# Kernel optimization log

Hardware: AMD Instinct MI355X
Metric: run time of the kernel (lower is better)

## Reference

```python
import jax, jax.numpy as jnp
import numpy as np

IN_F = 4096
OUT_F = 4096
GROUPSIZE = 128
NUM_GROUPS = IN_F // GROUPSIZE  # 32


def setup_inputs() -> dict:
    key = jax.random.key(0)
    k1, k2, k3, k4 = jax.random.split(key, 4)
    x = jax.random.normal(k1, (4, 2048, IN_F), dtype=jnp.float32)
    imin = jnp.iinfo(jnp.int32).min
    imax = jnp.iinfo(jnp.int32).max
    qweight = jax.random.randint(k2, (IN_F // 8, OUT_F), imin, imax, dtype=jnp.int32)
    qzeros = jax.random.randint(k3, (NUM_GROUPS, OUT_F // 8), imin, imax, dtype=jnp.int32)
    scales = jax.random.uniform(k4, (NUM_GROUPS, OUT_F), dtype=jnp.float32,
                                minval=1e-3, maxval=2e-2)
    return {"x": x, "qweight": qweight, "qzeros": qzeros, "scales": scales}


def _unpack_rows(q):
    # q: int32 [in/8, out] -> float nibbles [in, out]; nibble i of a word is bits 4i..4i+3
    u = q.astype(jnp.uint32)
    shifts = (4 * jnp.arange(8, dtype=jnp.uint32))[None, :, None]  # [1,8,1]
    nib = (u[:, None, :] >> shifts) & jnp.uint32(0xF)              # [in/8, 8, out]
    return nib.reshape(q.shape[0] * 8, q.shape[1]).astype(jnp.float32)


def _unpack_cols(q):
    # q: int32 [g, out/8] -> float nibbles [g, out]
    u = q.astype(jnp.uint32)
    shifts = (4 * jnp.arange(8, dtype=jnp.uint32))[None, None, :]  # [1,1,8]
    nib = (u[:, :, None] >> shifts) & jnp.uint32(0xF)              # [g, out/8, 8]
    return nib.reshape(q.shape[0], q.shape[1] * 8).astype(jnp.float32)


def _dequant(qweight, qzeros, scales):
    # GPTQ dequant: w = scale[g] * (q - (z[g] + 1))
    q = _unpack_rows(qweight)                      # [IN_F, OUT_F]
    z = _unpack_cols(qzeros) + 1.0                 # [G, OUT_F]
    qg = q.reshape(NUM_GROUPS, GROUPSIZE, OUT_F)
    w = (qg - z[:, None, :]) * scales[:, None, :]
    return w.reshape(IN_F, OUT_F)


def reference(x, qweight, qzeros, scales):
    w = _dequant(qweight, qzeros, scales)          # [IN_F, OUT_F]
    # x: [B, S, IN_F] @ w -> [B, S, OUT_F]
    return jnp.einsum('bsi,io->bso', x, w)
```

## Files before the change

kernel.cpp:

```cpp
#include <hip/hip_runtime.h>
#include <stdint.h>

#define IN_F   4096
#define OUT_F  4096
#define M_ROWS 8192
#define KT     (IN_F / 64)

typedef __attribute__((ext_vector_type(8))) short  bf16x8;
typedef __attribute__((ext_vector_type(4))) float  f32x4;

__device__ __forceinline__ short f2bf(float f) {
    union { float f; uint32_t u; } v; v.f = f;
    uint32_t r = v.u + 0x7FFFu + ((v.u >> 16) & 1u);
    return (short)(r >> 16);
}

__device__ __forceinline__ void load_lds16(const void* gsrc, void* lds) {
    __builtin_amdgcn_global_load_lds(
        (const __attribute__((address_space(1))) uint32_t*)gsrc,
        (__attribute__((address_space(3))) uint32_t*)lds,
        16, 0, 0);
}

#define DQ_BLOCKS ((OUT_F * (IN_F / 8)) / 256)
#define XC_BLOCKS ((M_ROWS * IN_F / 8) / 256)

__global__ void prepass_kernel(const int* __restrict__ qweight,
                               const int* __restrict__ qzeros,
                               const float* __restrict__ scales,
                               const float* __restrict__ x,
                               short* __restrict__ wt,
                               short* __restrict__ xb)
{
    const int bid = blockIdx.x;
    if (bid < DQ_BLOCKS) {
        int t  = bid * 256 + threadIdx.x;
        int n  = t >> 9;
        int kw = t & 511;
        int g  = kw >> 4;

        float s = scales[g * OUT_F + n];
        uint32_t zw = (uint32_t)qzeros[g * (OUT_F / 8) + (n >> 3)];
        float z1 = (float)((zw >> (4 * (n & 7))) & 0xFu) + 1.0f;
        uint32_t q = (uint32_t)qweight[kw * OUT_F + n];

        bf16x8 out;
#pragma unroll
        for (int i = 0; i < 8; ++i) {
            float w = s * ((float)((q >> (4 * i)) & 0xFu) - z1);
            out[i] = f2bf(w);
        }
        *reinterpret_cast<bf16x8*>(&wt[(size_t)n * IN_F + kw * 8]) = out;
    } else {
        int t = (bid - DQ_BLOCKS) * 256 + threadIdx.x;
        const float4* src = reinterpret_cast<const float4*>(x) + (size_t)t * 2;
        float4 a = src[0], b = src[1];
        bf16x8 h;
        h[0] = f2bf(a.x); h[1] = f2bf(a.y); h[2] = f2bf(a.z); h[3] = f2bf(a.w);
        h[4] = f2bf(b.x); h[5] = f2bf(b.y); h[6] = f2bf(b.z); h[7] = f2bf(b.w);
        reinterpret_cast<bf16x8*>(xb)[t] = h;
    }
}

#define A_SLOT 32768
#define B_SLOT 32768

__global__ __launch_bounds__(512, 1) void gemm8_kernel(
    const short* __restrict__ Xb,
    const short* __restrict__ WT,
    float* __restrict__ C)
{
    __shared__ short AsBuf[3 * 256 * 64];
    __shared__ short BsBuf[2 * 256 * 64];
    char* const Abase = (char*)AsBuf;
    char* const Bbase = (char*)BsBuf;

    const int tid  = threadIdx.x;
    const int lane = tid & 63;
    const int wid  = tid >> 6;
    const int wr   = wid >> 2;
    const int wc   = wid & 3;

    const int row0 = blockIdx.y * 256;
    const int col0 = blockIdx.x * 256;

    const int rL0 = tid >> 3;
    const int csw = ((tid & 7) << 3) ^ ((rL0 & 7) << 3);
    const short* gA[4]; const short* gB[4]; int dOff[4];
#pragma unroll
    for (int L = 0; L < 4; ++L) {
        const int r = L * 64 + rL0;
        gA[L] = Xb + (size_t)(row0 + r) * IN_F + csw;
        gB[L] = WT + (size_t)(col0 + r) * IN_F + csw;
        dOff[L] = L * 8192 + tid * 16;
    }

    const int frow = lane & 15;
    const int k0   = ((lane >> 4) << 4) ^ ((frow & 7) << 4);

    f32x4 acc[8][4] = {};

#pragma unroll
    for (int L = 0; L < 4; ++L) load_lds16(gA[L],      Abase + 0 * A_SLOT + dOff[L]);
#pragma unroll
    for (int L = 0; L < 4; ++L) load_lds16(gB[L],      Bbase + 0 * B_SLOT + dOff[L]);
#pragma unroll
    for (int L = 0; L < 4; ++L) load_lds16(gA[L] + 64, Abase + 1 * A_SLOT + dOff[L]);
    asm volatile("s_waitcnt vmcnt(4)" ::: "memory");
    __builtin_amdgcn_s_barrier();

    int sA = 0;
    int sB = 0;

    for (int t = 0; t < KT; ++t) {
        char* Ab = Abase + sA * A_SLOT;
        char* Bb = Bbase + sB * B_SLOT;
        const int sA2 = (sA >= 1) ? sA - 1 : 2;
        char* An = Abase + sA2 * A_SLOT;
        char* Bn = Bbase + (sB ^ 1) * B_SLOT;
        const bool pfB = (t + 1 < KT);
        const bool pfA = (t + 2 < KT);

#pragma unroll
        for (int ks = 0; ks < 2; ++ks) {
            const int kb = k0 ^ (ks << 6);

            bf16x8 af[8]; bf16x8 bfr[4];
#pragma unroll
            for (int m = 0; m < 8; ++m) {
                const int r = wr * 128 + m * 16 + frow;
                af[m] = *reinterpret_cast<const bf16x8*>(Ab + r * 128 + kb);
            }
#pragma unroll
            for (int n = 0; n < 4; ++n) {
                const int r = wc * 64 + n * 16 + frow;
                bfr[n] = *reinterpret_cast<const bf16x8*>(Bb + r * 128 + kb);
            }

            if (ks == 0) {
                if (pfB) {
#pragma unroll
                    for (int L = 0; L < 4; ++L)
                        load_lds16(gB[L] + (size_t)(t + 1) * 64, Bn + dOff[L]);
                }
                if (pfA) {
#pragma unroll
                    for (int L = 0; L < 4; ++L)
                        load_lds16(gA[L] + (size_t)(t + 2) * 64, An + dOff[L]);
                }
            }

            __builtin_amdgcn_s_setprio(1);
#pragma unroll
            for (int m = 0; m < 8; ++m)
#pragma unroll
                for (int n = 0; n < 4; ++n)
                    acc[m][n] = __builtin_amdgcn_mfma_f32_16x16x32_bf16(
                        af[m], bfr[n], acc[m][n], 0, 0, 0);
            __builtin_amdgcn_s_setprio(0);
        }

        if (t < KT - 2)       asm volatile("s_waitcnt vmcnt(4)" ::: "memory");
        else if (t == KT - 2) asm volatile("s_waitcnt vmcnt(0)" ::: "memory");
        __builtin_amdgcn_s_barrier();

        sA = (sA < 2) ? sA + 1 : 0;
        sB ^= 1;
    }

    const int crow = (lane >> 4) * 4;
    const int ccol = lane & 15;
#pragma unroll
    for (int fm = 0; fm < 8; ++fm)
#pragma unroll
        for (int fn = 0; fn < 4; ++fn)
#pragma unroll
            for (int r = 0; r < 4; ++r) {
                const int row = row0 + wr * 128 + fm * 16 + crow + r;
                const int col = col0 + wc * 64 + fn * 16 + ccol;
                C[(size_t)row * OUT_F + col] = acc[fm][fn][r];
            }
}

#define BM 128
#define BN 128
#define BK 64

__global__ __launch_bounds__(256, 2) void gemm_x_wt_kernel(
    const float* __restrict__ X,
    const short* __restrict__ WT,
    float* __restrict__ C)
{
    __shared__ short As2[BM * BK];
    __shared__ short Bs2[BN * BK];

    const int bn = blockIdx.x;
    const int bm = blockIdx.y;
    const int tid  = threadIdx.x;
    const int lane = tid & 63;
    const int wid  = tid >> 6;
    const int wr   = wid >> 1;
    const int wc   = wid & 1;

    const int row0 = bm * BM;
    const int col0 = bn * BN;
    const int frow = lane & 15;
    const int fk   = (lane >> 4) * 8;

    f32x4 acc[4][4] = {};

    for (int kt = 0; kt < IN_F / BK; ++kt) {
        float4 a0[4], a1[4];
#pragma unroll
        for (int j = 0; j < 4; ++j) {
            const int flat = (j * 256 + tid) * 8;
            const int r = flat >> 6;
            const int c = flat & (BK - 1);
            const float* src = X + (size_t)(row0 + r) * IN_F + kt * BK + c;
            a0[j] = *reinterpret_cast<const float4*>(src);
            a1[j] = *reinterpret_cast<const float4*>(src + 4);
        }
        __syncthreads();
#pragma unroll
        for (int j = 0; j < 4; ++j) {
            const int flat = (j * 256 + tid) * 8;
            const int r = flat >> 6;
            const int c = flat & (BK - 1);
            load_lds16(WT + (size_t)(col0 + r) * IN_F + kt * BK + c, &Bs2[flat]);
        }
#pragma unroll
        for (int j = 0; j < 4; ++j) {
            const int flat = (j * 256 + tid) * 8;
            bf16x8 h;
            h[0] = f2bf(a0[j].x); h[1] = f2bf(a0[j].y);
            h[2] = f2bf(a0[j].z); h[3] = f2bf(a0[j].w);
            h[4] = f2bf(a1[j].x); h[5] = f2bf(a1[j].y);
            h[6] = f2bf(a1[j].z); h[7] = f2bf(a1[j].w);
            *reinterpret_cast<bf16x8*>(&As2[flat]) = h;
        }
        __syncthreads();
#pragma unroll
        for (int s = 0; s < 2; ++s) {
            bf16x8 af[4], bfr[4];
#pragma unroll
            for (int m = 0; m < 4; ++m) {
                const int row = wr * 64 + m * 16 + frow;
                af[m] = *reinterpret_cast<const bf16x8*>(&As2[row * BK + s * 32 + fk]);
            }
#pragma unroll
            for (int n = 0; n < 4; ++n) {
                const int col = wc * 64 + n * 16 + frow;
                bfr[n] = *reinterpret_cast<const bf16x8*>(&Bs2[col * BK + s * 32 + fk]);
            }
#pragma unroll
            for (int m = 0; m < 4; ++m)
#pragma unroll
                for (int n = 0; n < 4; ++n)
                    acc[m][n] = __builtin_amdgcn_mfma_f32_16x16x32_bf16(
                        af[m], bfr[n], acc[m][n], 0, 0, 0);
        }
    }

    const int crow = (lane >> 4) * 4;
    const int ccol = lane & 15;
#pragma unroll
    for (int m = 0; m < 4; ++m)
#pragma unroll
        for (int n = 0; n < 4; ++n)
#pragma unroll
            for (int r = 0; r < 4; ++r) {
                const int row = row0 + wr * 64 + m * 16 + crow + r;
                const int col = col0 + wc * 64 + n * 16 + ccol;
                C[(size_t)row * OUT_F + col] = acc[m][n][r];
            }
}

extern "C" void kernel_launch(void* const* d_in, const int* in_sizes, int n_in,
                              void* d_out, int out_size, void* d_ws, size_t ws_size,
                              hipStream_t stream) {
    const float* x       = (const float*)d_in[0];
    const int*   qweight = (const int*)  d_in[1];
    const int*   qzeros  = (const int*)  d_in[2];
    const float* scales  = (const float*)d_in[3];
    float*       out     = (float*)d_out;

    const size_t WT_BYTES = (size_t)OUT_F * IN_F * 2;
    const size_t XB_BYTES = (size_t)M_ROWS * IN_F * 2;

    short* wt = (short*)d_ws;

    if (ws_size >= WT_BYTES + XB_BYTES) {
        short* xb = (short*)((char*)d_ws + WT_BYTES);
        prepass_kernel<<<DQ_BLOCKS + XC_BLOCKS, 256, 0, stream>>>(
            qweight, qzeros, scales, x, wt, xb);
        dim3 grid(OUT_F / 256, M_ROWS / 256);
        gemm8_kernel<<<grid, 512, 0, stream>>>(xb, wt, out);
    } else {
        prepass_kernel<<<DQ_BLOCKS, 256, 0, stream>>>(
            qweight, qzeros, scales, x, wt, (short*)nullptr);
        dim3 grid(OUT_F / BN, M_ROWS / BM);
        gemm_x_wt_kernel<<<grid, 256, 0, stream>>>(x, wt, out);
    }
}
```

Baseline: 272.0 us.

## Split MFMA k-step into half-tiles with interleaved prefetch and extra barriers

Each k-substep is split into two halves of four M-fragments. Every half first reads its fragments from LDS, then issues two of the global-to-LDS prefetch loads and runs 16 MFMAs. The B prefetch is issued in ks=0 and the A prefetch in ks=1, spreading memory issue across the loop instead of bursting it once. This lowers live fragment registers and tries a ping-pong schedule between waves, at the cost of four barriers per substep, which may add synchronisation stalls.

```diff
diff --git a/kernel.cpp b/kernel.cpp
--- a/kernel.cpp
+++ b/kernel.cpp
@@ -121,48 +121,88 @@
         const bool pfB = (t + 1 < KT);
         const bool pfA = (t + 2 < KT);
 
+        bf16x8 bfr[4];
+
 #pragma unroll
         for (int ks = 0; ks < 2; ++ks) {
             const int kb = k0 ^ (ks << 6);
 
-            bf16x8 af[8]; bf16x8 bfr[4];
-#pragma unroll
-            for (int m = 0; m < 8; ++m) {
-                const int r = wr * 128 + m * 16 + frow;
-                af[m] = *reinterpret_cast<const bf16x8*>(Ab + r * 128 + kb);
-            }
-#pragma unroll
-            for (int n = 0; n < 4; ++n) {
-                const int r = wc * 64 + n * 16 + frow;
-                bfr[n] = *reinterpret_cast<const bf16x8*>(Bb + r * 128 + kb);
-            }
-
-            if (ks == 0) {
-                if (pfB) {
-#pragma unroll
-                    for (int L = 0; L < 4; ++L)
-                        load_lds16(gB[L] + (size_t)(t + 1) * 64, Bn + dOff[L]);
-                }
-                if (pfA) {
-#pragma unroll
-                    for (int L = 0; L < 4; ++L)
-                        load_lds16(gA[L] + (size_t)(t + 2) * 64, An + dOff[L]);
-                }
-            }
-
-            __builtin_amdgcn_s_setprio(1);
-#pragma unroll
-            for (int m = 0; m < 8; ++m)
-#pragma unroll
-                for (int n = 0; n < 4; ++n)
-                    acc[m][n] = __builtin_amdgcn_mfma_f32_16x16x32_bf16(
-                        af[m], bfr[n], acc[m][n], 0, 0, 0);
-            __builtin_amdgcn_s_setprio(0);
-        }
-
-        if (t < KT - 2)       asm volatile("s_waitcnt vmcnt(4)" ::: "memory");
-        else if (t == KT - 2) asm volatile("s_waitcnt vmcnt(0)" ::: "memory");
-        __builtin_amdgcn_s_barrier();
+            {
+                bf16x8 af[4];
+#pragma unroll
+                for (int m = 0; m < 4; ++m) {
+                    const int r = wr * 128 + m * 16 + frow;
+                    af[m] = *reinterpret_cast<const bf16x8*>(Ab + r * 128 + kb);
+                }
+#pragma unroll
+                for (int n = 0; n < 4; ++n) {
+                    const int r = wc * 64 + n * 16 + frow;
+                    bfr[n] = *reinterpret_cast<const bf16x8*>(Bb + r * 128 + kb);
+                }
+                if (ks == 0) {
+                    if (pfB) {
+                        load_lds16(gB[0] + (size_t)(t + 1) * 64, Bn + dOff[0]);
+                        load_lds16(gB[1] + (size_t)(t + 1) * 64, Bn + dOff[1]);
+                    }
+                } else {
+                    if (pfA) {
+                        load_lds16(gA[0] + (size_t)(t + 2) * 64, An + dOff[0]);
+                        load_lds16(gA[1] + (size_t)(t + 2) * 64, An + dOff[1]);
+                    }
+                }
+
+                __builtin_amdgcn_s_barrier();
+                asm volatile("s_waitcnt lgkmcnt(0)" ::: "memory");
+                __builtin_amdgcn_s_setprio(1);
+#pragma unroll
+                for (int m = 0; m < 4; ++m)
+#pragma unroll
+                    for (int n = 0; n < 4; ++n)
+                        acc[m][n] = __builtin_amdgcn_mfma_f32_16x16x32_bf16(
+                            af[m], bfr[n], acc[m][n], 0, 0, 0);
+                __builtin_amdgcn_s_setprio(0);
+                __builtin_amdgcn_s_barrier();
+            }
+
+            {
+                bf16x8 ag[4];
+#pragma unroll
+                for (int m = 0; m < 4; ++m) {
+                    const int r = wr * 128 + (m + 4) * 16 + frow;
+                    ag[m] = *reinterpret_cast<const bf16x8*>(Ab + r * 128 + kb);
+                }
+                if (ks == 0) {
+                    if (pfB) {
+                        load_lds16(gB[2] + (size_t)(t + 1) * 64, Bn + dOff[2]);
+                        load_lds16(gB[3] + (size_t)(t + 1) * 64, Bn + dOff[3]);
+                    }
+                } else {
+                    if (pfA) {
+                        load_lds16(gA[2] + (size_t)(t + 2) * 64, An + dOff[2]);
+                        load_lds16(gA[3] + (size_t)(t + 2) * 64, An + dOff[3]);
+                    }
+                }
+
+                __builtin_amdgcn_s_barrier();
+                asm volatile("s_waitcnt lgkmcnt(0)" ::: "memory");
+                __builtin_amdgcn_s_setprio(1);
+#pragma unroll
+                for (int m = 0; m < 4; ++m)
+#pragma unroll
+                    for (int n = 0; n < 4; ++n)
+                        acc[m + 4][n] = __builtin_amdgcn_mfma_f32_16x16x32_bf16(
+                            ag[m], bfr[n], acc[m + 4][n], 0, 0, 0);
+                __builtin_amdgcn_s_setprio(0);
+
+                if (ks == 1) {
+                    if (t < KT - 2)
+                        asm volatile("s_waitcnt vmcnt(4)" ::: "memory");
+                    else if (t == KT - 2)
+                        asm volatile("s_waitcnt vmcnt(0)" ::: "memory");
+                }
+                __builtin_amdgcn_s_barrier();
+            }
+        }
 
         sA = (sA < 2) ? sA + 1 : 0;
         sB ^= 1;
```

Measured after the change: 282.6 us. 1.04x slower.
